# Optimization experiments

Measured on AMD Instinct MI355X. Metric: run time of the kernel, lower is better.

Reference implementation:

```python
import jax, jax.numpy as jnp
import numpy as np

D_MODEL = 1024
NHEAD = 16
D_K = D_MODEL // NHEAD


def sparsemax(z):
    # sparsemax along last axis (Martins & Astudillo 2016)
    n = z.shape[-1]
    z_sorted = jnp.flip(jnp.sort(z, axis=-1), axis=-1)          # descending
    k = jnp.arange(1, n + 1, dtype=z.dtype)
    z_cumsum = jnp.cumsum(z_sorted, axis=-1)
    support = (1.0 + k * z_sorted) > z_cumsum                    # [..., n] bool
    k_max = jnp.sum(support, axis=-1, keepdims=True)             # [..., 1] int
    tau_sum = jnp.take_along_axis(z_cumsum, k_max - 1, axis=-1)
    tau = (tau_sum - 1.0) / k_max.astype(z.dtype)
    return jnp.maximum(z - tau, 0.0)


def setup_inputs() -> dict:
    key = jax.random.key(0)
    ks = jax.random.split(key, 12)
    B, S = 2, 2048
    s = 1.0 / np.sqrt(D_MODEL)
    inp = {
        'query': jax.random.normal(ks[0], (B, S, D_MODEL), jnp.float32),
        'key':   jax.random.normal(ks[1], (B, S, D_MODEL), jnp.float32),
        'value': jax.random.normal(ks[2], (B, S, D_MODEL), jnp.float32),
        'Wq': jax.random.uniform(ks[3], (D_MODEL, D_MODEL), jnp.float32, -s, s),
        'bq': jax.random.uniform(ks[4], (D_MODEL,), jnp.float32, -s, s),
        'Wk': jax.random.uniform(ks[5], (D_MODEL, D_MODEL), jnp.float32, -s, s),
        'bk': jax.random.uniform(ks[6], (D_MODEL,), jnp.float32, -s, s),
        'Wv': jax.random.uniform(ks[7], (D_MODEL, D_MODEL), jnp.float32, -s, s),
        'bv': jax.random.uniform(ks[8], (D_MODEL,), jnp.float32, -s, s),
        'Wfc': jax.random.uniform(ks[9], (D_MODEL, D_MODEL), jnp.float32, -s, s),
        'bfc': jax.random.uniform(ks[10], (D_MODEL,), jnp.float32, -s, s),
    }
    return inp


def reference(query, key, value, Wq, bq, Wk, bk, Wv, bv, Wfc, bfc):
    B, S, _ = query.shape
    # projections (torch Linear: x @ W.T + b)
    q = (query @ Wq.T + bq).reshape(B, S, NHEAD, D_K).transpose(0, 2, 1, 3)
    k = (key   @ Wk.T + bk).reshape(B, S, NHEAD, D_K).transpose(0, 2, 1, 3)
    v = (value @ Wv.T + bv).reshape(B, S, NHEAD, D_K).transpose(0, 2, 1, 3)
    # scaled dot-product with sparsemax
    logits = jnp.einsum('bhqd,bhkd->bhqk', q, k) / np.sqrt(D_K).astype(jnp.float32)
    attention = sparsemax(logits)                                # [B,H,S,S]
    attn_out = jnp.einsum('bhqk,bhkd->bhqd', attention, v)
    attn_out = attn_out.transpose(0, 2, 1, 3).reshape(B, S, D_MODEL)
    output = attn_out @ Wfc.T + bfc                              # dropout = identity (eval)
    return output, attention
```

## Files before the change

### kernel.cpp

```cpp
#include <hip/hip_runtime.h>
#include <hip/hip_bf16.h>
#include <cstdint>

#define S_LEN  2048
#define DMODEL 1024
#define NHEAD  16
#define M_ROWS 4096

typedef __attribute__((ext_vector_type(8))) short bf16x8;
typedef __attribute__((ext_vector_type(4))) float f32x4;

__device__ __forceinline__ unsigned short f2bf(float f) {
    __hip_bfloat16 h = __float2bfloat16(f);
    return __builtin_bit_cast(unsigned short, h);
}
__device__ __forceinline__ float bf2f(unsigned short u) {
    return __builtin_bit_cast(float, (unsigned)u << 16);
}
__device__ __forceinline__ uint4 pack8(float4 a, float4 b) {
    uint4 u;
    u.x = ((unsigned)f2bf(a.y) << 16) | f2bf(a.x);
    u.y = ((unsigned)f2bf(a.w) << 16) | f2bf(a.z);
    u.z = ((unsigned)f2bf(b.y) << 16) | f2bf(b.x);
    u.w = ((unsigned)f2bf(b.w) << 16) | f2bf(b.z);
    return u;
}

__device__ __forceinline__ float wave_sum64(float v) {
    v += __shfl_xor(v, 32, 64); v += __shfl_xor(v, 16, 64);
    v += __shfl_xor(v, 8, 64);  v += __shfl_xor(v, 4, 64);
    v += __shfl_xor(v, 2, 64);  v += __shfl_xor(v, 1, 64);
    return v;
}
__device__ __forceinline__ float wave_max64(float v) {
    v = fmaxf(v, __shfl_xor(v, 32, 64)); v = fmaxf(v, __shfl_xor(v, 16, 64));
    v = fmaxf(v, __shfl_xor(v, 8, 64));  v = fmaxf(v, __shfl_xor(v, 4, 64));
    v = fmaxf(v, __shfl_xor(v, 2, 64));  v = fmaxf(v, __shfl_xor(v, 1, 64));
    return v;
}
__device__ __forceinline__ int lanes_below(unsigned long long m) {
    return __builtin_amdgcn_mbcnt_hi((unsigned)(m >> 32),
           __builtin_amdgcn_mbcnt_lo((unsigned)m, 0));
}

__global__ __launch_bounds__(256)
void qkv_gemm(const float* __restrict__ xq, const float* __restrict__ xk,
              const float* __restrict__ xv,
              const float* __restrict__ Wq, const float* __restrict__ Wk,
              const float* __restrict__ Wv,
              const float* __restrict__ bq, const float* __restrict__ bk,
              const float* __restrict__ bv,
              unsigned short* __restrict__ Q_bf, unsigned short* __restrict__ K_bf,
              unsigned short* __restrict__ V_bf) {
    const int which = blockIdx.z;
    const float* A    = (which == 0) ? xq : (which == 1) ? xk : xv;
    const float* W    = (which == 0) ? Wq : (which == 1) ? Wk : Wv;
    const float* bias = (which == 0) ? bq : (which == 1) ? bk : bv;
    unsigned short* dst = (which == 0) ? Q_bf : (which == 1) ? K_bf : V_bf;
    const float qscale = (which == 0) ? 0.125f : 1.0f;

    const int row0 = blockIdx.x * 128;
    const int col0 = blockIdx.y * 128;

    __shared__ unsigned short SMEM[10240];
    unsigned short* As = SMEM;
    unsigned short* Bs = SMEM + 5120;

    const int t = threadIdx.x;
    const int wid = t >> 6, lane = t & 63;
    const int wm = wid >> 1, wn = wid & 1;
    const int l = lane & 15, quad = lane >> 4;

    f32x4 acc[4][4];
#pragma unroll
    for (int i = 0; i < 4; ++i)
#pragma unroll
        for (int j = 0; j < 4; ++j) {
            float b_ = bias[col0 + wn * 64 + j * 16 + l];
            acc[i][j] = (f32x4){ b_, b_, b_, b_ };
        }

    for (int k0 = 0; k0 < DMODEL; k0 += 32) {
        uint4 ar[2], br[2];
#pragma unroll
        for (int i = 0; i < 2; ++i) {
            const int c = t + i * 256, r = c >> 2, q = (c & 3) * 8;
            const float* ap = A + (size_t)(row0 + r) * DMODEL + k0 + q;
            const float* wp = W + (size_t)(col0 + r) * DMODEL + k0 + q;
            float4 a0 = *(const float4*)ap, a1 = *(const float4*)(ap + 4);
            float4 w0 = *(const float4*)wp, w1 = *(const float4*)(wp + 4);
            ar[i] = pack8(a0, a1);
            br[i] = pack8(w0, w1);
        }
        __syncthreads();
#pragma unroll
        for (int i = 0; i < 2; ++i) {
            const int c = t + i * 256, r = c >> 2, q = (c & 3) * 8;
            *(uint4*)&As[r * 40 + q] = ar[i];
            *(uint4*)&Bs[r * 40 + q] = br[i];
        }
        __syncthreads();
        bf16x8 a[4], b[4];
#pragma unroll
        for (int i = 0; i < 4; ++i)
            a[i] = *(const bf16x8*)&As[(wm * 64 + i * 16 + l) * 40 + quad * 8];
#pragma unroll
        for (int j = 0; j < 4; ++j)
            b[j] = *(const bf16x8*)&Bs[(wn * 64 + j * 16 + l) * 40 + quad * 8];
#pragma unroll
        for (int i = 0; i < 4; ++i)
#pragma unroll
            for (int j = 0; j < 4; ++j)
                acc[i][j] = __builtin_amdgcn_mfma_f32_16x16x32_bf16(a[i], b[j], acc[i][j], 0, 0, 0);
    }

    __syncthreads();
    unsigned short* Cs = SMEM;
#pragma unroll 1
    for (int jh = 0; jh < 2; ++jh) {
        if (wn == jh) {
#pragma unroll
            for (int i = 0; i < 4; ++i)
#pragma unroll
                for (int j = 0; j < 4; ++j)
#pragma unroll
                    for (int r = 0; r < 4; ++r)
                        Cs[(wm * 64 + i * 16 + quad * 4 + r) * 72 + j * 16 + l] =
                            f2bf(acc[i][j][r] * qscale);
        }
        __syncthreads();
#pragma unroll
        for (int it = 0; it < 4; ++it) {
            const int idx = t + it * 256;
            const int row = idx >> 3, c8 = (idx & 7) * 8;
            *(uint4*)(dst + (size_t)(row0 + row) * DMODEL + col0 + jh * 64 + c8) =
                *(const uint4*)&Cs[row * 72 + c8];
        }
        __syncthreads();
    }
}

__global__ __launch_bounds__(512, 6)
void attn_fused(const unsigned short* __restrict__ Q_bf,
                const unsigned short* __restrict__ K_bf,
                const unsigned short* __restrict__ V_bf,
                float* __restrict__ attn,
                unsigned short* __restrict__ AO_bf) {
    const int t = threadIdx.x;
    const int w = t >> 6, lane = t & 63;
    const int l = lane & 15, quad = lane >> 4;
    const int bh = blockIdx.y, b_ = bh >> 4, h = bh & 15;
    const int r0 = blockIdx.x * 8;

    __shared__ uint2 List[8 * 512];
    float* LDSf = (float*)List;

    const unsigned short* Qp =
        Q_bf + ((size_t)(b_ * S_LEN + r0 + (l & 7))) * DMODEL + h * 64 + quad * 8;
    const bf16x8 a0 = *(const bf16x8*)Qp;
    const bf16x8 a1 = *(const bf16x8*)(Qp + 32);

    float z[32];
    float m = -__builtin_inff();
#pragma unroll
    for (int q = 0; q < 4; ++q) {
        const unsigned short* Kb =
            K_bf + ((size_t)(b_ * S_LEN + q * 512 + w * 64 + l)) * DMODEL
            + h * 64 + quad * 8;
        f32x4 acc[4];
#pragma unroll
        for (int ct = 0; ct < 4; ++ct) {
            const unsigned short* Kp = Kb + (size_t)(ct * 16) * DMODEL;
            const bf16x8 b0 = *(const bf16x8*)Kp;
            const bf16x8 b1 = *(const bf16x8*)(Kp + 32);
            f32x4 c = {};
            c = __builtin_amdgcn_mfma_f32_16x16x32_bf16(a0, b0, c, 0, 0, 0);
            c = __builtin_amdgcn_mfma_f32_16x16x32_bf16(a1, b1, c, 0, 0, 0);
            acc[ct] = c;
        }
        if (quad < 2) {
#pragma unroll
            for (int ct = 0; ct < 4; ++ct)
#pragma unroll
                for (int r = 0; r < 4; ++r)
                    LDSf[(quad * 4 + r) * 512 + w * 64 + ct * 16 + l] = acc[ct][r];
        }
        __syncthreads();
#pragma unroll
        for (int j = 0; j < 8; ++j) {
            z[q * 8 + j] = LDSf[w * 512 + j * 64 + lane];
            m = fmaxf(m, z[q * 8 + j]);
        }
        __syncthreads();
    }

    m = wave_max64(m);

    float tau = m - 1.0f;
#pragma unroll 1
    for (int it = 0; it < 10; ++it) {
        float ss = 0.0f;
        int kk = 0;
#pragma unroll
        for (int j = 0; j < 32; ++j) {
            const bool c = z[j] > tau;
            kk += (int)__popcll(__ballot(c));
            ss += c ? z[j] : 0.0f;
        }
        ss = wave_sum64(ss);
        const float tn = (ss - 1.0f) / (float)kk;
        if (tn == tau) break;
        tau = tn;
    }

    uint2* list = List + w * 512;
    float* ap = attn + (size_t)bh * S_LEN * S_LEN + (size_t)(r0 + w) * S_LEN;
    int scnt = 0;
#pragma unroll
    for (int jj = 0; jj < 32; ++jj) {
        const float pv = fmaxf(z[jj] - tau, 0.0f);
        __builtin_nontemporal_store(pv, ap + (jj >> 3) * 512 + (jj & 7) * 64 + lane);
        const unsigned long long mk = __ballot(pv > 0.0f);
        if (pv > 0.0f) {
            const int pos = scnt + lanes_below(mk);
            if (pos < 480)
                list[pos] = (uint2){ (unsigned)((jj >> 3) * 512 + (jj & 7) * 64 + lane),
                                     __builtin_bit_cast(unsigned, pv) };
        }
        scnt += (int)__popcll(mk);
    }
    if (scnt > 480) scnt = 480;

    if (lane < 32)
        list[scnt + lane] = (uint2){ 0u, 0u };

    const unsigned short* Vh = V_bf + ((size_t)b_ * S_LEN) * DMODEL + h * 64;
    const int sub = lane >> 3, dbase = (lane & 7) * 8;
    float acc8[8] = {};
    const int gmax4 = (scnt + 31) >> 5;
#pragma unroll 1
    for (int g = 0; g < gmax4; ++g) {
        const int b0 = g * 32 + sub;
        const uint2 e0 = list[b0];
        const uint2 e1 = list[b0 + 8];
        const uint2 e2 = list[b0 + 16];
        const uint2 e3 = list[b0 + 24];
        const uint4 v0 = *(const uint4*)(Vh + (size_t)e0.x * DMODEL + dbase);
        const uint4 v1 = *(const uint4*)(Vh + (size_t)e1.x * DMODEL + dbase);
        const uint4 v2 = *(const uint4*)(Vh + (size_t)e2.x * DMODEL + dbase);
        const uint4 v3 = *(const uint4*)(Vh + (size_t)e3.x * DMODEL + dbase);
        const float p0 = __builtin_bit_cast(float, e0.y);
        const float p1 = __builtin_bit_cast(float, e1.y);
        const float p2 = __builtin_bit_cast(float, e2.y);
        const float p3 = __builtin_bit_cast(float, e3.y);
        acc8[0] += p0 * bf2f((unsigned short)(v0.x & 0xffff));
        acc8[1] += p0 * bf2f((unsigned short)(v0.x >> 16));
        acc8[2] += p0 * bf2f((unsigned short)(v0.y & 0xffff));
        acc8[3] += p0 * bf2f((unsigned short)(v0.y >> 16));
        acc8[4] += p0 * bf2f((unsigned short)(v0.z & 0xffff));
        acc8[5] += p0 * bf2f((unsigned short)(v0.z >> 16));
        acc8[6] += p0 * bf2f((unsigned short)(v0.w & 0xffff));
        acc8[7] += p0 * bf2f((unsigned short)(v0.w >> 16));
        acc8[0] += p1 * bf2f((unsigned short)(v1.x & 0xffff));
        acc8[1] += p1 * bf2f((unsigned short)(v1.x >> 16));
        acc8[2] += p1 * bf2f((unsigned short)(v1.y & 0xffff));
        acc8[3] += p1 * bf2f((unsigned short)(v1.y >> 16));
        acc8[4] += p1 * bf2f((unsigned short)(v1.z & 0xffff));
        acc8[5] += p1 * bf2f((unsigned short)(v1.z >> 16));
        acc8[6] += p1 * bf2f((unsigned short)(v1.w & 0xffff));
        acc8[7] += p1 * bf2f((unsigned short)(v1.w >> 16));
        acc8[0] += p2 * bf2f((unsigned short)(v2.x & 0xffff));
        acc8[1] += p2 * bf2f((unsigned short)(v2.x >> 16));
        acc8[2] += p2 * bf2f((unsigned short)(v2.y & 0xffff));
        acc8[3] += p2 * bf2f((unsigned short)(v2.y >> 16));
        acc8[4] += p2 * bf2f((unsigned short)(v2.z & 0xffff));
        acc8[5] += p2 * bf2f((unsigned short)(v2.z >> 16));
        acc8[6] += p2 * bf2f((unsigned short)(v2.w & 0xffff));
        acc8[7] += p2 * bf2f((unsigned short)(v2.w >> 16));
        acc8[0] += p3 * bf2f((unsigned short)(v3.x & 0xffff));
        acc8[1] += p3 * bf2f((unsigned short)(v3.x >> 16));
        acc8[2] += p3 * bf2f((unsigned short)(v3.y & 0xffff));
        acc8[3] += p3 * bf2f((unsigned short)(v3.y >> 16));
        acc8[4] += p3 * bf2f((unsigned short)(v3.z & 0xffff));
        acc8[5] += p3 * bf2f((unsigned short)(v3.z >> 16));
        acc8[6] += p3 * bf2f((unsigned short)(v3.w & 0xffff));
        acc8[7] += p3 * bf2f((unsigned short)(v3.w >> 16));
    }
#pragma unroll
    for (int d = 0; d < 8; ++d) {
        acc8[d] += __shfl_xor(acc8[d], 8, 64);
        acc8[d] += __shfl_xor(acc8[d], 16, 64);
        acc8[d] += __shfl_xor(acc8[d], 32, 64);
    }
    if (lane < 8) {
        union { unsigned short u[8]; uint4 v; } o;
#pragma unroll
        for (int d = 0; d < 8; ++d) o.u[d] = f2bf(acc8[d]);
        *(uint4*)(AO_bf + ((size_t)(b_ * S_LEN + r0 + w)) * DMODEL
                  + h * 64 + lane * 8) = o.v;
    }
}

__global__ __launch_bounds__(256)
void fc_gemm(const unsigned short* __restrict__ AO_bf,
             const float* __restrict__ Wfc,
             const float* __restrict__ bfc, float* __restrict__ out) {
    const int row0 = blockIdx.x * 128;
    const int col0 = blockIdx.y * 128;

    __shared__ unsigned short As[128 * 40];
    __shared__ unsigned short Bs[128 * 40];

    const int t = threadIdx.x;
    const int wid = t >> 6, lane = t & 63;
    const int wm = wid >> 1, wn = wid & 1;
    const int l = lane & 15, quad = lane >> 4;

    f32x4 acc[4][4];
#pragma unroll
    for (int i = 0; i < 4; ++i)
#pragma unroll
        for (int j = 0; j < 4; ++j) {
            float b_ = bfc[col0 + wn * 64 + j * 16 + l];
            acc[i][j] = (f32x4){ b_, b_, b_, b_ };
        }

    for (int k0 = 0; k0 < DMODEL; k0 += 32) {
        uint4 ar[2], br[2];
#pragma unroll
        for (int i = 0; i < 2; ++i) {
            const int c = t + i * 256, r = c >> 2, q = (c & 3) * 8;
            ar[i] = *(const uint4*)(AO_bf + (size_t)(row0 + r) * DMODEL + k0 + q);
            const float* wp = Wfc + (size_t)(col0 + r) * DMODEL + k0 + q;
            float4 w0 = *(const float4*)wp, w1 = *(const float4*)(wp + 4);
            br[i] = pack8(w0, w1);
        }
        __syncthreads();
#pragma unroll
        for (int i = 0; i < 2; ++i) {
            const int c = t + i * 256, r = c >> 2, q = (c & 3) * 8;
            *(uint4*)&As[r * 40 + q] = ar[i];
            *(uint4*)&Bs[r * 40 + q] = br[i];
        }
        __syncthreads();
        bf16x8 a[4], b[4];
#pragma unroll
        for (int i = 0; i < 4; ++i)
            a[i] = *(const bf16x8*)&As[(wm * 64 + i * 16 + l) * 40 + quad * 8];
#pragma unroll
        for (int j = 0; j < 4; ++j)
            b[j] = *(const bf16x8*)&Bs[(wn * 64 + j * 16 + l) * 40 + quad * 8];
#pragma unroll
        for (int i = 0; i < 4; ++i)
#pragma unroll
            for (int j = 0; j < 4; ++j)
                acc[i][j] = __builtin_amdgcn_mfma_f32_16x16x32_bf16(a[i], b[j], acc[i][j], 0, 0, 0);
    }

#pragma unroll
    for (int i = 0; i < 4; ++i)
#pragma unroll
        for (int r = 0; r < 4; ++r) {
            const int m = row0 + wm * 64 + i * 16 + quad * 4 + r;
#pragma unroll
            for (int j = 0; j < 4; ++j) {
                const int n = col0 + wn * 64 + j * 16 + l;
                out[(size_t)m * DMODEL + n] = acc[i][j][r];
            }
        }
}

extern "C" void kernel_launch(void* const* d_in, const int* in_sizes, int n_in,
                              void* d_out, int out_size, void* d_ws, size_t ws_size,
                              hipStream_t stream) {
    const float* q   = (const float*)d_in[0];
    const float* k   = (const float*)d_in[1];
    const float* v   = (const float*)d_in[2];
    const float* Wq  = (const float*)d_in[3];
    const float* bq  = (const float*)d_in[4];
    const float* Wk  = (const float*)d_in[5];
    const float* bk  = (const float*)d_in[6];
    const float* Wv  = (const float*)d_in[7];
    const float* bv  = (const float*)d_in[8];
    const float* Wfc = (const float*)d_in[9];
    const float* bfc = (const float*)d_in[10];

    float* out  = (float*)d_out;
    float* attn = out + (size_t)M_ROWS * DMODEL;

    char* ws = (char*)d_ws;
    unsigned short* Q_bf  = (unsigned short*)ws;
    unsigned short* K_bf  = (unsigned short*)(ws + (8u << 20));
    unsigned short* V_bf  = (unsigned short*)(ws + (16u << 20));
    unsigned short* AO_bf = (unsigned short*)(ws + (24u << 20));

    qkv_gemm<<<dim3(32, 8, 3), 256, 0, stream>>>(q, k, v, Wq, Wk, Wv,
                                                  bq, bk, bv, Q_bf, K_bf, V_bf);
    attn_fused<<<dim3(S_LEN / 8, 32), 512, 0, stream>>>(Q_bf, K_bf, V_bf, attn, AO_bf);
    fc_gemm<<<dim3(32, 8), 256, 0, stream>>>(AO_bf, Wfc, bfc, out);
}
```

Before: 890.3 us.

## Double-buffer GEMM tiles, widen attention blocks, compact sparsemax candidates

Both GEMMs gain register-prefetch double buffering, so the next K-slice global loads overlap the MFMA work and one barrier per iteration is removed. The attention kernel now handles 16 query rows per 1024-thread block, so each K tile load feeds all 16 MFMA rows instead of 8 duplicated ones. It prefetches the next K chunk into registers and double-buffers the LDS transpose. Sparsemax does one full pass, then compacts the candidates above tau into a short list and iterates only over those, with a fallback when there are more than 256. These changes raise register and LDS pressure and lower occupancy per block.

New measurement: 794.8 us. 1.12x faster.

```diff
diff --git a/kernel.cpp b/kernel.cpp
--- a/kernel.cpp
+++ b/kernel.cpp
@@ -62,10 +62,7 @@
     const int row0 = blockIdx.x * 128;
     const int col0 = blockIdx.y * 128;
 
-    __shared__ unsigned short SMEM[10240];
-    unsigned short* As = SMEM;
-    unsigned short* Bs = SMEM + 5120;
-
+    __shared__ unsigned short SMEM[20480];
     const int t = threadIdx.x;
     const int wid = t >> 6, lane = t & 63;
     const int wm = wid >> 1, wn = wid & 1;
@@ -80,19 +77,21 @@
             acc[i][j] = (f32x4){ b_, b_, b_, b_ };
         }
 
+    uint4 ar[2], br[2];
+#pragma unroll
+    for (int i = 0; i < 2; ++i) {
+        const int c = t + i * 256, r = c >> 2, q = (c & 3) * 8;
+        const float* ap = A + (size_t)(row0 + r) * DMODEL + q;
+        const float* wp = W + (size_t)(col0 + r) * DMODEL + q;
+        float4 a0 = *(const float4*)ap, a1 = *(const float4*)(ap + 4);
+        float4 w0 = *(const float4*)wp, w1 = *(const float4*)(wp + 4);
+        ar[i] = pack8(a0, a1);
+        br[i] = pack8(w0, w1);
+    }
+
     for (int k0 = 0; k0 < DMODEL; k0 += 32) {
-        uint4 ar[2], br[2];
-#pragma unroll
-        for (int i = 0; i < 2; ++i) {
-            const int c = t + i * 256, r = c >> 2, q = (c & 3) * 8;
-            const float* ap = A + (size_t)(row0 + r) * DMODEL + k0 + q;
-            const float* wp = W + (size_t)(col0 + r) * DMODEL + k0 + q;
-            float4 a0 = *(const float4*)ap, a1 = *(const float4*)(ap + 4);
-            float4 w0 = *(const float4*)wp, w1 = *(const float4*)(wp + 4);
-            ar[i] = pack8(a0, a1);
-            br[i] = pack8(w0, w1);
-        }
-        __syncthreads();
+        unsigned short* As = SMEM + ((k0 >> 5) & 1) * 10240;
+        unsigned short* Bs = As + 5120;
 #pragma unroll
         for (int i = 0; i < 2; ++i) {
             const int c = t + i * 256, r = c >> 2, q = (c & 3) * 8;
@@ -100,6 +99,18 @@
             *(uint4*)&Bs[r * 40 + q] = br[i];
         }
         __syncthreads();
+        if (k0 + 32 < DMODEL) {
+#pragma unroll
+            for (int i = 0; i < 2; ++i) {
+                const int c = t + i * 256, r = c >> 2, q = (c & 3) * 8;
+                const float* ap = A + (size_t)(row0 + r) * DMODEL + k0 + 32 + q;
+                const float* wp = W + (size_t)(col0 + r) * DMODEL + k0 + 32 + q;
+                float4 a0 = *(const float4*)ap, a1 = *(const float4*)(ap + 4);
+                float4 w0 = *(const float4*)wp, w1 = *(const float4*)(wp + 4);
+                ar[i] = pack8(a0, a1);
+                br[i] = pack8(w0, w1);
+            }
+        }
         bf16x8 a[4], b[4];
 #pragma unroll
         for (int i = 0; i < 4; ++i)
@@ -140,7 +151,7 @@
     }
 }
 
-__global__ __launch_bounds__(512, 6)
+__global__ __launch_bounds__(1024, 4)
 void attn_fused(const unsigned short* __restrict__ Q_bf,
                 const unsigned short* __restrict__ K_bf,
                 const unsigned short* __restrict__ V_bf,
@@ -150,57 +161,65 @@
     const int w = t >> 6, lane = t & 63;
     const int l = lane & 15, quad = lane >> 4;
     const int bh = blockIdx.y, b_ = bh >> 4, h = bh & 15;
-    const int r0 = blockIdx.x * 8;
-
-    __shared__ uint2 List[8 * 512];
-    float* LDSf = (float*)List;
+    const int r0 = blockIdx.x * 16;
+
+    __shared__ float TR[2][16][516];
+    uint2* List = (uint2*)&TR[0][0][0];
 
     const unsigned short* Qp =
-        Q_bf + ((size_t)(b_ * S_LEN + r0 + (l & 7))) * DMODEL + h * 64 + quad * 8;
+        Q_bf + ((size_t)(b_ * S_LEN + r0 + l)) * DMODEL + h * 64 + quad * 8;
     const bf16x8 a0 = *(const bf16x8*)Qp;
     const bf16x8 a1 = *(const bf16x8*)(Qp + 32);
 
+    const unsigned short* KB =
+        K_bf + ((size_t)(b_ * S_LEN + w * 32 + l)) * DMODEL + h * 64 + quad * 8;
+
     float z[32];
     float m = -__builtin_inff();
+    bf16x8 cb0[2], cb1[2], nb0[2], nb1[2];
+#pragma unroll
+    for (int ct = 0; ct < 2; ++ct) {
+        const unsigned short* Kp = KB + (size_t)(ct * 16) * DMODEL;
+        cb0[ct] = *(const bf16x8*)Kp;
+        cb1[ct] = *(const bf16x8*)(Kp + 32);
+    }
 #pragma unroll
     for (int q = 0; q < 4; ++q) {
-        const unsigned short* Kb =
-            K_bf + ((size_t)(b_ * S_LEN + q * 512 + w * 64 + l)) * DMODEL
-            + h * 64 + quad * 8;
-        f32x4 acc[4];
-#pragma unroll
-        for (int ct = 0; ct < 4; ++ct) {
-            const unsigned short* Kp = Kb + (size_t)(ct * 16) * DMODEL;
-            const bf16x8 b0 = *(const bf16x8*)Kp;
-            const bf16x8 b1 = *(const bf16x8*)(Kp + 32);
+        if (q < 3) {
+#pragma unroll
+            for (int ct = 0; ct < 2; ++ct) {
+                const unsigned short* Kp =
+                    KB + (size_t)((q + 1) * 512 + ct * 16) * DMODEL;
+                nb0[ct] = *(const bf16x8*)Kp;
+                nb1[ct] = *(const bf16x8*)(Kp + 32);
+            }
+        }
+#pragma unroll
+        for (int ct = 0; ct < 2; ++ct) {
             f32x4 c = {};
-            c = __builtin_amdgcn_mfma_f32_16x16x32_bf16(a0, b0, c, 0, 0, 0);
-            c = __builtin_amdgcn_mfma_f32_16x16x32_bf16(a1, b1, c, 0, 0, 0);
-            acc[ct] = c;
-        }
-        if (quad < 2) {
-#pragma unroll
-            for (int ct = 0; ct < 4; ++ct)
-#pragma unroll
-                for (int r = 0; r < 4; ++r)
-                    LDSf[(quad * 4 + r) * 512 + w * 64 + ct * 16 + l] = acc[ct][r];
+            c = __builtin_amdgcn_mfma_f32_16x16x32_bf16(a0, cb0[ct], c, 0, 0, 0);
+            c = __builtin_amdgcn_mfma_f32_16x16x32_bf16(a1, cb1[ct], c, 0, 0, 0);
+#pragma unroll
+            for (int r = 0; r < 4; ++r)
+                TR[q & 1][quad * 4 + r][w * 32 + ct * 16 + l] = c[r];
         }
         __syncthreads();
 #pragma unroll
         for (int j = 0; j < 8; ++j) {
-            z[q * 8 + j] = LDSf[w * 512 + j * 64 + lane];
+            z[q * 8 + j] = TR[q & 1][w][j * 64 + lane];
             m = fmaxf(m, z[q * 8 + j]);
         }
-        __syncthreads();
-    }
+        if (q < 3) {
+#pragma unroll
+            for (int ct = 0; ct < 2; ++ct) { cb0[ct] = nb0[ct]; cb1[ct] = nb1[ct]; }
+        }
+    }
+    __syncthreads();
 
     m = wave_max64(m);
-
     float tau = m - 1.0f;
-#pragma unroll 1
-    for (int it = 0; it < 10; ++it) {
-        float ss = 0.0f;
-        int kk = 0;
+    {
+        float ss = 0.0f; int kk = 0;
 #pragma unroll
         for (int j = 0; j < 32; ++j) {
             const bool c = z[j] > tau;
@@ -208,28 +227,100 @@
             ss += c ? z[j] : 0.0f;
         }
         ss = wave_sum64(ss);
-        const float tn = (ss - 1.0f) / (float)kk;
-        if (tn == tau) break;
-        tau = tn;
+        tau = (ss - 1.0f) / (float)kk;
     }
 
     uint2* list = List + w * 512;
+    int cnt = 0;
+#pragma unroll
+    for (int jj = 0; jj < 32; ++jj) {
+        const float zv = z[jj];
+        const unsigned long long mk = __ballot(zv > tau);
+        if (zv > tau) {
+            const int pos = cnt + lanes_below(mk);
+            if (pos < 512)
+                list[pos] = (uint2){ (unsigned)((jj >> 3) * 512 + (jj & 7) * 64 + lane),
+                                     __builtin_bit_cast(unsigned, zv) };
+        }
+        cnt += (int)__popcll(mk);
+    }
+
+    int scnt = 0;
+    if (cnt <= 256) {
+        const float NEG = -__builtin_inff();
+        const uint2 E0 = list[lane];
+        const uint2 E1 = list[64 + lane];
+        const uint2 E2 = list[128 + lane];
+        const uint2 E3 = list[192 + lane];
+        const float zc0 = (lane < cnt)       ? __builtin_bit_cast(float, E0.y) : NEG;
+        const float zc1 = (64 + lane < cnt)  ? __builtin_bit_cast(float, E1.y) : NEG;
+        const float zc2 = (128 + lane < cnt) ? __builtin_bit_cast(float, E2.y) : NEG;
+        const float zc3 = (192 + lane < cnt) ? __builtin_bit_cast(float, E3.y) : NEG;
+#pragma unroll 1
+        for (int it = 0; it < 12; ++it) {
+            float ss = 0.0f; int kk = 0;
+            kk += (int)__popcll(__ballot(zc0 > tau)); ss += (zc0 > tau) ? zc0 : 0.0f;
+            kk += (int)__popcll(__ballot(zc1 > tau)); ss += (zc1 > tau) ? zc1 : 0.0f;
+            kk += (int)__popcll(__ballot(zc2 > tau)); ss += (zc2 > tau) ? zc2 : 0.0f;
+            kk += (int)__popcll(__ballot(zc3 > tau)); ss += (zc3 > tau) ? zc3 : 0.0f;
+            ss = wave_sum64(ss);
+            const float tn = (ss - 1.0f) / (float)kk;
+            if (tn == tau) break;
+            tau = tn;
+        }
+        unsigned long long mk;
+        mk = __ballot(zc0 > tau);
+        if (zc0 > tau) list[scnt + lanes_below(mk)] =
+            (uint2){ E0.x, __builtin_bit_cast(unsigned, zc0 - tau) };
+        scnt += (int)__popcll(mk);
+        mk = __ballot(zc1 > tau);
+        if (zc1 > tau) list[scnt + lanes_below(mk)] =
+            (uint2){ E1.x, __builtin_bit_cast(unsigned, zc1 - tau) };
+        scnt += (int)__popcll(mk);
+        mk = __ballot(zc2 > tau);
+        if (zc2 > tau) list[scnt + lanes_below(mk)] =
+            (uint2){ E2.x, __builtin_bit_cast(unsigned, zc2 - tau) };
+        scnt += (int)__popcll(mk);
+        mk = __ballot(zc3 > tau);
+        if (zc3 > tau) list[scnt + lanes_below(mk)] =
+            (uint2){ E3.x, __builtin_bit_cast(unsigned, zc3 - tau) };
+        scnt += (int)__popcll(mk);
+    } else {
+#pragma unroll 1
+        for (int it = 0; it < 9; ++it) {
+            float ss = 0.0f; int kk = 0;
+#pragma unroll
+            for (int j = 0; j < 32; ++j) {
+                const bool c = z[j] > tau;
+                kk += (int)__popcll(__ballot(c));
+                ss += c ? z[j] : 0.0f;
+            }
+            ss = wave_sum64(ss);
+            const float tn = (ss - 1.0f) / (float)kk;
+            if (tn == tau) break;
+            tau = tn;
+        }
+#pragma unroll
+        for (int jj = 0; jj < 32; ++jj) {
+            const float zv = z[jj];
+            const unsigned long long mk = __ballot(zv > tau);
+            if (zv > tau) {
+                const int pos = scnt + lanes_below(mk);
+                if (pos < 480)
+                    list[pos] = (uint2){ (unsigned)((jj >> 3) * 512 + (jj & 7) * 64 + lane),
+                                         __builtin_bit_cast(unsigned, zv - tau) };
+            }
+            scnt += (int)__popcll(mk);
+        }
+        if (scnt > 480) scnt = 480;
+    }
+
     float* ap = attn + (size_t)bh * S_LEN * S_LEN + (size_t)(r0 + w) * S_LEN;
-    int scnt = 0;
 #pragma unroll
     for (int jj = 0; jj < 32; ++jj) {
         const float pv = fmaxf(z[jj] - tau, 0.0f);
         __builtin_nontemporal_store(pv, ap + (jj >> 3) * 512 + (jj & 7) * 64 + lane);
-        const unsigned long long mk = __ballot(pv > 0.0f);
-        if (pv > 0.0f) {
-            const int pos = scnt + lanes_below(mk);
-            if (pos < 480)
-                list[pos] = (uint2){ (unsigned)((jj >> 3) * 512 + (jj & 7) * 64 + lane),
-                                     __builtin_bit_cast(unsigned, pv) };
-        }
-        scnt += (int)__popcll(mk);
-    }
-    if (scnt > 480) scnt = 480;
+    }
 
     if (lane < 32)
         list[scnt + lane] = (uint2){ 0u, 0u };
@@ -308,8 +399,7 @@
     const int row0 = blockIdx.x * 128;
     const int col0 = blockIdx.y * 128;
 
-    __shared__ unsigned short As[128 * 40];
-    __shared__ unsigned short Bs[128 * 40];
+    __shared__ unsigned short SMEM[20480];
 
     const int t = threadIdx.x;
     const int wid = t >> 6, lane = t & 63;
@@ -325,17 +415,19 @@
             acc[i][j] = (f32x4){ b_, b_, b_, b_ };
         }
 
+    uint4 ar[2], br[2];
+#pragma unroll
+    for (int i = 0; i < 2; ++i) {
+        const int c = t + i * 256, r = c >> 2, q = (c & 3) * 8;
+        ar[i] = *(const uint4*)(AO_bf + (size_t)(row0 + r) * DMODEL + q);
+        const float* wp = Wfc + (size_t)(col0 + r) * DMODEL + q;
+        float4 w0 = *(const float4*)wp, w1 = *(const float4*)(wp + 4);
+        br[i] = pack8(w0, w1);
+    }
+
     for (int k0 = 0; k0 < DMODEL; k0 += 32) {
-        uint4 ar[2], br[2];
-#pragma unroll
-        for (int i = 0; i < 2; ++i) {
-            const int c = t + i * 256, r = c >> 2, q = (c & 3) * 8;
-            ar[i] = *(const uint4*)(AO_bf + (size_t)(row0 + r) * DMODEL + k0 + q);
-            const float* wp = Wfc + (size_t)(col0 + r) * DMODEL + k0 + q;
-            float4 w0 = *(const float4*)wp, w1 = *(const float4*)(wp + 4);
-            br[i] = pack8(w0, w1);
-        }
-        __syncthreads();
+        unsigned short* As = SMEM + ((k0 >> 5) & 1) * 10240;
+        unsigned short* Bs = As + 5120;
 #pragma unroll
         for (int i = 0; i < 2; ++i) {
             const int c = t + i * 256, r = c >> 2, q = (c & 3) * 8;
@@ -343,6 +435,16 @@
             *(uint4*)&Bs[r * 40 + q] = br[i];
         }
         __syncthreads();
+        if (k0 + 32 < DMODEL) {
+#pragma unroll
+            for (int i = 0; i < 2; ++i) {
+                const int c = t + i * 256, r = c >> 2, q = (c & 3) * 8;
+                ar[i] = *(const uint4*)(AO_bf + (size_t)(row0 + r) * DMODEL + k0 + 32 + q);
+                const float* wp = Wfc + (size_t)(col0 + r) * DMODEL + k0 + 32 + q;
+                float4 w0 = *(const float4*)wp, w1 = *(const float4*)(wp + 4);
+                br[i] = pack8(w0, w1);
+            }
+        }
         bf16x8 a[4], b[4];
 #pragma unroll
         for (int i = 0; i < 4; ++i)
@@ -396,6 +498,6 @@
 
     qkv_gemm<<<dim3(32, 8, 3), 256, 0, stream>>>(q, k, v, Wq, Wk, Wv,
                                                   bq, bk, bv, Q_bf, K_bf, V_bf);
-    attn_fused<<<dim3(S_LEN / 8, 32), 512, 0, stream>>>(Q_bf, K_bf, V_bf, attn, AO_bf);
+    attn_fused<<<dim3(S_LEN / 16, 32), 1024, 0, stream>>>(Q_bf, K_bf, V_bf, attn, AO_bf);
     fc_gemm<<<dim3(32, 8), 256, 0, stream>>>(AO_bf, Wfc, bfc, out);
 }
```
